# Kernel optimization log

Measured on AMD Instinct MI355X. Metric: run time of the kernel, lower is better.

The kernel has to match this reference:

```python
import jax, jax.numpy as jnp
import numpy as np

BS, T, FIN, FOUT = 8, 1024, 512, 512
ALPHA = 0.1      # leaky relu slope
T_K = 3          # t_ksize (odd); temporal band radius = T_K // 2
S_K = 4          # s_ksize semantic topk
NEG_INF = -9e15


def setup_inputs() -> dict:
    key = jax.random.key(0)
    k1, k2, k3, k4 = jax.random.split(key, 4)
    # xavier-uniform-ish scales (gain 1.414)
    w_lim = 1.414 * np.sqrt(6.0 / (FIN + FOUT))
    a_lim = 1.414 * np.sqrt(6.0 / (2 * FOUT + 1))
    return {
        "x_a": jax.random.normal(k1, (BS, T, FIN), jnp.float32),
        "x_v": jax.random.normal(k2, (BS, T, FIN), jnp.float32),
        "W": jax.random.uniform(k3, (FIN, FOUT), jnp.float32, -w_lim, w_lim),
        "a": jax.random.uniform(k4, (2 * FOUT, 1), jnp.float32, -a_lim, a_lim),
    }


def _temporal_mask(t):
    # tem_adj[i,j] = 1 iff |i-j| <= T_K//2 and i, j on the same side of t-0.5
    idx = jnp.arange(2 * t)
    same_side = (idx[:, None] >= t) == (idx[None, :] >= t)
    band = jnp.abs(idx[:, None] - idx[None, :]) <= (T_K // 2)
    return band & same_side  # (2t, 2t) bool


def _semantic_block_mask(x, k):
    # x: (bs, t, d). Top-k neighbors by negative squared euclidean distance.
    inner = 2.0 * jnp.einsum("btd,bsd->bts", x, x)
    sq = jnp.sum(x * x, axis=-1, keepdims=True)  # (bs, t, 1)
    pd = -(sq - inner + jnp.swapaxes(sq, -1, -2))  # (bs, t, t)
    _, idx = jax.lax.top_k(pd, k)  # (bs, t, k)
    bs, t = x.shape[0], x.shape[1]
    b_ix = jnp.arange(bs)[:, None, None]
    r_ix = jnp.arange(t)[None, :, None]
    return jnp.zeros((bs, t, t), bool).at[b_ix, r_ix, idx].set(True)


def reference(x_a, x_v, W, a):
    bs, t, _ = x_a.shape
    h = jnp.concatenate([x_a, x_v], axis=1)          # (bs, 2t, FIN)
    Wh = h @ W                                        # (bs, 2t, FOUT)

    # additive GAT score: e = leakyrelu(Wh a1 + (Wh a2)^T)
    Wh1 = Wh @ a[:FOUT]                               # (bs, 2t, 1)
    Wh2 = Wh @ a[FOUT:]                               # (bs, 2t, 1)
    e = Wh1 + jnp.swapaxes(Wh2, -1, -2)               # (bs, 2t, 2t)
    e = jnp.where(e > 0, e, ALPHA * e)                # leaky relu

    # adjacency: temporal band + semantic topk within aa / vv blocks
    tem = _temporal_mask(t)                           # (2t, 2t)
    sem_aa = _semantic_block_mask(Wh[:, :t], S_K)     # (bs, t, t)
    sem_vv = _semantic_block_mask(Wh[:, t:], S_K)     # (bs, t, t)
    zb = jnp.zeros((bs, t, t), bool)
    sem = jnp.concatenate([
        jnp.concatenate([sem_aa, zb], axis=-1),
        jnp.concatenate([zb, sem_vv], axis=-1),
    ], axis=1)                                        # (bs, 2t, 2t)
    mask = tem[None] | sem

    attention = jax.nn.softmax(jnp.where(mask, e, NEG_INF), axis=-1)
    h_prime = jax.nn.elu(attention @ Wh)              # (bs, 2t, FOUT)
    return h_prime[:, :t], h_prime[:, t:]
```

## Files before the change

### kernel.cpp

```cpp
#include <hip/hip_runtime.h>
#include <math.h>

#define T_ 1024
#define BS_ 8
#define D_ 512
#define NROWS_ (BS_*2*T_)
#define ALPHA_ 0.1f

typedef _Float16 f16;
typedef _Float16 f16x8 __attribute__((ext_vector_type(8)));
typedef _Float16 f16x4 __attribute__((ext_vector_type(4)));
typedef float f32x4 __attribute__((ext_vector_type(4)));

#define MFMA16(A,B,C) __builtin_amdgcn_mfma_f32_16x16x32_f16((A),(B),(C),0,0,0)

__device__ __forceinline__ void gl16(const void* g, void* l) {
    __builtin_amdgcn_global_load_lds(
        (const __attribute__((address_space(1))) unsigned int*)g,
        (__attribute__((address_space(3))) unsigned int*)l, 16, 0, 0);
}

__device__ __forceinline__ unsigned sortable(float f) {
    unsigned u = __float_as_uint(f);
    return u ^ ((u & 0x80000000u) ? 0xFFFFFFFFu : 0x80000000u);
}
__device__ __forceinline__ unsigned pack_key(float s, int col) {
    return (sortable(s) & 0xFFFFFC00u) | (unsigned)(1023 - col);
}

#define INSK4(K, X) { \
    bool g3 = (X) > K[3], g2 = (X) > K[2], g1 = (X) > K[1], g0 = (X) > K[0]; \
    K[3] = g2 ? K[2] : (g3 ? (X) : K[3]); \
    K[2] = g1 ? K[1] : (g2 ? (X) : K[2]); \
    K[1] = g0 ? K[0] : (g1 ? (X) : K[1]); \
    K[0] = g0 ? (X) : K[0]; }

#define INSK8(K, X) { \
    bool h7=(X)>K[7],h6=(X)>K[6],h5=(X)>K[5],h4=(X)>K[4]; \
    bool h3=(X)>K[3],h2=(X)>K[2],h1=(X)>K[1],h0=(X)>K[0]; \
    K[7]=h6?K[6]:(h7?(X):K[7]); K[6]=h5?K[5]:(h6?(X):K[6]); \
    K[5]=h4?K[4]:(h5?(X):K[5]); K[4]=h3?K[3]:(h4?(X):K[4]); \
    K[3]=h2?K[2]:(h3?(X):K[3]); K[2]=h1?K[1]:(h2?(X):K[2]); \
    K[1]=h0?K[0]:(h1?(X):K[1]); K[0]=h0?(X):K[0]; }

#define CEU(a,b) { unsigned mx_ = (a) > (b) ? (a) : (b); \
    unsigned mn_ = (a) > (b) ? (b) : (a); (a) = mx_; (b) = mn_; }

#define MERGE8(K, MSK) { \
    unsigned b0=__shfl_xor(K[0],MSK), b1=__shfl_xor(K[1],MSK), \
             b2=__shfl_xor(K[2],MSK), b3=__shfl_xor(K[3],MSK), \
             b4=__shfl_xor(K[4],MSK), b5=__shfl_xor(K[5],MSK), \
             b6=__shfl_xor(K[6],MSK), b7=__shfl_xor(K[7],MSK); \
    K[0]=K[0]>b7?K[0]:b7; K[1]=K[1]>b6?K[1]:b6; \
    K[2]=K[2]>b5?K[2]:b5; K[3]=K[3]>b4?K[3]:b4; \
    K[4]=K[4]>b3?K[4]:b3; K[5]=K[5]>b2?K[5]:b2; \
    K[6]=K[6]>b1?K[6]:b1; K[7]=K[7]>b0?K[7]:b0; \
    CEU(K[0],K[4]); CEU(K[1],K[5]); CEU(K[2],K[6]); CEU(K[3],K[7]); \
    CEU(K[0],K[2]); CEU(K[1],K[3]); CEU(K[4],K[6]); CEU(K[5],K[7]); \
    CEU(K[0],K[1]); CEU(K[2],K[3]); CEU(K[4],K[5]); CEU(K[6],K[7]); }

#define BETTER(x,xi,v,vi) ((x) > (v) || ((x) == (v) && (xi) < (vi)))
#define INS4T(TV,TI,X,ID) { \
    bool g3 = BETTER(X,ID,TV[3],TI[3]), g2 = BETTER(X,ID,TV[2],TI[2]); \
    bool g1 = BETTER(X,ID,TV[1],TI[1]), g0 = BETTER(X,ID,TV[0],TI[0]); \
    TV[3] = g2 ? TV[2] : (g3 ? (X) : TV[3]); TI[3] = g2 ? TI[2] : (g3 ? (ID) : TI[3]); \
    TV[2] = g1 ? TV[1] : (g2 ? (X) : TV[2]); TI[2] = g1 ? TI[1] : (g2 ? (ID) : TI[2]); \
    TV[1] = g0 ? TV[0] : (g1 ? (X) : TV[1]); TI[1] = g0 ? TI[0] : (g1 ? (ID) : TI[1]); \
    TV[0] = g0 ? (X) : TV[0]; TI[0] = g0 ? (ID) : TI[0]; }

__global__ __launch_bounds__(256) void k_splitW(
    const float* __restrict__ W, f16* __restrict__ WTh, f16* __restrict__ WTl)
{
    __shared__ float tile[64][65];
    const int tid = threadIdx.x;
    const int tk = (blockIdx.x >> 3) << 6, tn = (blockIdx.x & 7) << 6;
    const int r0 = tid >> 4, c4 = (tid & 15) << 2;

    #pragma unroll
    for (int rr = 0; rr < 4; ++rr) {
        int k = r0 + (rr << 4);
        float4 v = *(const float4*)(W + (size_t)(tk + k) * D_ + tn + c4);
        tile[k][c4+0] = v.x; tile[k][c4+1] = v.y;
        tile[k][c4+2] = v.z; tile[k][c4+3] = v.w;
    }
    __syncthreads();
    #pragma unroll
    for (int rr = 0; rr < 4; ++rr) {
        int n = r0 + (rr << 4);
        f16x4 h, l;
        #pragma unroll
        for (int i = 0; i < 4; ++i) {
            float x = tile[c4 + i][n];
            f16 hh = (f16)x; h[i] = hh; l[i] = (f16)(x - (float)hh);
        }
        *(f16x4*)(WTh + (size_t)(tn + n) * D_ + tk + c4) = h;
        *(f16x4*)(WTl + (size_t)(tn + n) * D_ + tk + c4) = l;
    }
}

#define SA_OFF 73728
#define ST_OFF 77824
__global__ __launch_bounds__(256) void k_gemm_wh(
    const float* __restrict__ xa, const float* __restrict__ xv,
    const f16* __restrict__ WTh, const f16* __restrict__ WTl,
    const float* __restrict__ a,
    f16* __restrict__ Whh, f16* __restrict__ Whl,
    float* __restrict__ Wh1, float* __restrict__ Wh2, float* __restrict__ sq)
{
    __shared__ __align__(16) unsigned char smem[79360];

    const int tid  = threadIdx.x;
    const int w    = tid >> 6;
    const int lane = tid & 63;
    const int l15  = lane & 15;
    const int g    = lane >> 4;
    const int rowbase = blockIdx.x << 5;

    const int r8  = lane >> 3;
    const int k7  = lane & 7;
    const int sw2 = ((k7 ^ r8) << 4);
    const int rowA = tid >> 3;
    const int k7A  = tid & 7;
    const int aswz = ((k7A ^ (rowA & 7)) << 4);

    const int q0x = (((lane >> 4) ^ (lane & 7)) << 4);
    const int aoff0 = 65536 + ((0  + l15) << 7) + q0x;
    const int aoff1 = 65536 + ((16 + l15) << 7) + q0x;
    const int boff0 = (((w << 6) +  0 + l15) << 7) + q0x;
    const int boff1 = (((w << 6) + 16 + l15) << 7) + q0x;
    const int boff2 = (((w << 6) + 32 + l15) << 7) + q0x;
    const int boff3 = (((w << 6) + 48 + l15) << 7) + q0x;

    *(float4*)(smem + SA_OFF + (tid << 4)) = *(const float4*)(a + (tid << 2));

    const int qp = rowbase >> 10;
    const float* srcA = ((qp & 1) ? xv : xa)
                      + (size_t)((qp >> 1) * 1024 + (rowbase & 1023) + rowA) * D_ + (k7A << 3);

    const char* WThB = (const char*)WTh;
    const char* WTlB = (const char*)WTl;

    float st1[8], st2[8], stq[8];
    #pragma unroll
    for (int s = 0; s < 8; ++s) { st1[s] = 0.f; st2[s] = 0.f; stq[s] = 0.f; }

    for (int ct = 0; ct < 2; ++ct) {
        const int colbase = ct << 8;
        f32x4 acc[2][4];
        #pragma unroll
        for (int m = 0; m < 2; ++m)
            #pragma unroll
            for (int c = 0; c < 4; ++c) acc[m][c] = (f32x4){0.f,0.f,0.f,0.f};

        for (int kc = 0; kc < 8; ++kc) {
            size_t gB = ((size_t)(colbase + (w << 6) + r8) << 10) + (kc << 7) + sw2;
            int ldsB = (w << 13) + (lane << 4);
            #pragma unroll
            for (int j = 0; j < 8; ++j) {
                gl16(WThB + gB, smem + ldsB);
                gl16(WTlB + gB, smem + 32768 + ldsB);
                gB += (size_t)8 << 10; ldsB += 1024;
            }
            {
                float4 v0 = *(const float4*)(srcA + (kc << 6));
                float4 v1 = *(const float4*)(srcA + (kc << 6) + 4);
                float xs[8] = {v0.x,v0.y,v0.z,v0.w,v1.x,v1.y,v1.z,v1.w};
                f16x8 hi, lo;
                #pragma unroll
                for (int e = 0; e < 8; ++e) {
                    f16 h = (f16)xs[e]; hi[e] = h; lo[e] = (f16)(xs[e] - (float)h);
                }
                const int ldsA = 65536 + (rowA << 7) + aswz;
                *(f16x8*)(smem + ldsA)        = hi;
                *(f16x8*)(smem + ldsA + 4096) = lo;
            }
            __syncthreads();

            #pragma unroll
            for (int s = 0; s < 2; ++s) {
                const int sx = s << 6;
                f16x8 ah0 = *(const f16x8*)(smem + (aoff0 ^ sx));
                f16x8 ah1 = *(const f16x8*)(smem + (aoff1 ^ sx));
                f16x8 al0 = *(const f16x8*)(smem + ((aoff0 ^ sx) + 4096));
                f16x8 al1 = *(const f16x8*)(smem + ((aoff1 ^ sx) + 4096));
                f16x8 bh0 = *(const f16x8*)(smem + (boff0 ^ sx));
                f16x8 bh1 = *(const f16x8*)(smem + (boff1 ^ sx));
                f16x8 bh2 = *(const f16x8*)(smem + (boff2 ^ sx));
                f16x8 bh3 = *(const f16x8*)(smem + (boff3 ^ sx));
                f16x8 bl0 = *(const f16x8*)(smem + ((boff0 ^ sx) + 32768));
                f16x8 bl1 = *(const f16x8*)(smem + ((boff1 ^ sx) + 32768));
                f16x8 bl2 = *(const f16x8*)(smem + ((boff2 ^ sx) + 32768));
                f16x8 bl3 = *(const f16x8*)(smem + ((boff3 ^ sx) + 32768));

                acc[0][0] = MFMA16(ah0, bh0, acc[0][0]);
                acc[0][1] = MFMA16(ah0, bh1, acc[0][1]);
                acc[0][2] = MFMA16(ah0, bh2, acc[0][2]);
                acc[0][3] = MFMA16(ah0, bh3, acc[0][3]);
                acc[1][0] = MFMA16(ah1, bh0, acc[1][0]);
                acc[1][1] = MFMA16(ah1, bh1, acc[1][1]);
                acc[1][2] = MFMA16(ah1, bh2, acc[1][2]);
                acc[1][3] = MFMA16(ah1, bh3, acc[1][3]);
                acc[0][0] = MFMA16(al0, bh0, acc[0][0]);
                acc[0][1] = MFMA16(al0, bh1, acc[0][1]);
                acc[0][2] = MFMA16(al0, bh2, acc[0][2]);
                acc[0][3] = MFMA16(al0, bh3, acc[0][3]);
                acc[1][0] = MFMA16(al1, bh0, acc[1][0]);
                acc[1][1] = MFMA16(al1, bh1, acc[1][1]);
                acc[1][2] = MFMA16(al1, bh2, acc[1][2]);
                acc[1][3] = MFMA16(al1, bh3, acc[1][3]);
                acc[0][0] = MFMA16(ah0, bl0, acc[0][0]);
                acc[0][1] = MFMA16(ah0, bl1, acc[0][1]);
                acc[0][2] = MFMA16(ah0, bl2, acc[0][2]);
                acc[0][3] = MFMA16(ah0, bl3, acc[0][3]);
                acc[1][0] = MFMA16(ah1, bl0, acc[1][0]);
                acc[1][1] = MFMA16(ah1, bl1, acc[1][1]);
                acc[1][2] = MFMA16(ah1, bl2, acc[1][2]);
                acc[1][3] = MFMA16(ah1, bl3, acc[1][3]);
            }
            __syncthreads();
        }

        #pragma unroll
        for (int c = 0; c < 4; ++c) {
            const int col = (ct << 8) + (w << 6) + (c << 4) + l15;
            const float a1 = *(const float*)(smem + SA_OFF + (col << 2));
            const float a2 = *(const float*)(smem + SA_OFF + 2048 + (col << 2));
            #pragma unroll
            for (int m = 0; m < 2; ++m)
                #pragma unroll
                for (int j = 0; j < 4; ++j) {
                    const float v = acc[m][c][j];
                    const int slot = (m << 2) + j;
                    st1[slot] = fmaf(v, a1, st1[slot]);
                    st2[slot] = fmaf(v, a2, st2[slot]);
                    stq[slot] = fmaf(v, v,  stq[slot]);
                    f16 h = (f16)v; f16 l = (f16)(v - (float)h);
                    const size_t off = (size_t)(rowbase + (m << 4) + (g << 2) + j) * D_ + col;
                    Whh[off] = h; Whl[off] = l;
                }
        }
    }

    #pragma unroll
    for (int mask = 1; mask < 16; mask <<= 1)
        #pragma unroll
        for (int s = 0; s < 8; ++s) {
            st1[s] += __shfl_xor(st1[s], mask);
            st2[s] += __shfl_xor(st2[s], mask);
            stq[s] += __shfl_xor(stq[s], mask);
        }
    if (l15 == 0) {
        #pragma unroll
        for (int s = 0; s < 8; ++s) {
            const int rl = ((s >> 2) << 4) + (g << 2) + (s & 3);
            float* sp = (float*)(smem + ST_OFF) + ((w << 5) + rl) * 3;
            sp[0] = st1[s]; sp[1] = st2[s]; sp[2] = stq[s];
        }
    }
    __syncthreads();
    if (tid < 32) {
        float s1 = 0.f, s2 = 0.f, s3 = 0.f;
        #pragma unroll
        for (int wv = 0; wv < 4; ++wv) {
            const float* sp = (const float*)(smem + ST_OFF) + ((wv << 5) + tid) * 3;
            s1 += sp[0]; s2 += sp[1]; s3 += sp[2];
        }
        Wh1[rowbase + tid] = s1; Wh2[rowbase + tid] = s2; sq[rowbase + tid] = s3;
    }
}

__global__ __launch_bounds__(512, 1) void k_gram_topk8(
    const f16* __restrict__ Whh, const float* __restrict__ sq,
    int* __restrict__ topk8)
{
    __shared__ __align__(16) unsigned char smem[81920];

    const int bid = blockIdx.x;
    const int swz = ((bid & 7) << 5) + (bid >> 3);
    const int p   = swz >> 4;
    const int rt  = swz & 15;
    const int rowbase  = (p << 10) + (rt << 6);
    const int colPanel = p << 10;

    const int tid  = threadIdx.x;
    const int w    = tid >> 6;
    const int wr   = w >> 2, wc = w & 3;
    const int lane = tid & 63;
    const int l15  = lane & 15;
    const int g    = lane >> 4;
    const int r8   = lane >> 3;
    const int k7   = lane & 7;
    const int sw2  = ((k7 ^ r8) << 4);
    const int q0x  = ((g ^ (lane & 7)) << 4);

    const int rowA = tid >> 3;
    const int k7A  = tid & 7;
    const int aswz = ((k7A ^ (rowA & 7)) << 4);

    const char* WB = (const char*)Whh;

    const int aoff0 = 32768 + (((wr << 5) +  0 + l15) << 7) + q0x;
    const int aoff1 = 32768 + (((wr << 5) + 16 + l15) << 7) + q0x;
    const int boff0 = (((wc << 6) +  0 + l15) << 7) + q0x;
    const int boff1 = (((wc << 6) + 16 + l15) << 7) + q0x;
    const int boff2 = (((wc << 6) + 32 + l15) << 7) + q0x;
    const int boff3 = (((wc << 6) + 48 + l15) << 7) + q0x;

    f32x4 acc[2][4];
    #pragma unroll
    for (int m = 0; m < 2; ++m)
        #pragma unroll
        for (int c = 0; c < 4; ++c) acc[m][c] = (f32x4){0.f,0.f,0.f,0.f};

    unsigned k4[8][4];
    #pragma unroll
    for (int s = 0; s < 8; ++s)
        #pragma unroll
        for (int q = 0; q < 4; ++q) k4[s][q] = 0u;

    #define STAGE_G(t) { \
        const int ct_ = (t) >> 3, kc_ = (t) & 7; \
        const int bufb_ = ((t) & 1) * 40960; \
        size_t gB_ = ((size_t)(colPanel + (ct_ << 8) + (w << 5) + r8) << 10) + (kc_ << 7) + sw2; \
        int ldsB_ = bufb_ + (w << 12) + (lane << 4); \
        _Pragma("unroll") \
        for (int j_ = 0; j_ < 4; ++j_) { \
            gl16(WB + gB_, smem + ldsB_); \
            gB_ += (size_t)8 << 10; ldsB_ += 1024; \
        } \
        size_t gA_ = ((size_t)(rowbase + rowA) << 10) + (kc_ << 7) + aswz; \
        gl16(WB + gA_, smem + bufb_ + 32768 + (tid << 4)); \
    }

    STAGE_G(0);

    for (int t = 0; t < 32; ++t) {
        __syncthreads();
        if (t < 31) STAGE_G(t + 1);
        const int bufb = (t & 1) * 40960;

        #pragma unroll
        for (int s = 0; s < 2; ++s) {
            const int sx = s << 6;
            f16x8 a0 = *(const f16x8*)(smem + bufb + (aoff0 ^ sx));
            f16x8 a1 = *(const f16x8*)(smem + bufb + (aoff1 ^ sx));
            f16x8 b0 = *(const f16x8*)(smem + bufb + (boff0 ^ sx));
            f16x8 b1 = *(const f16x8*)(smem + bufb + (boff1 ^ sx));
            f16x8 b2 = *(const f16x8*)(smem + bufb + (boff2 ^ sx));
            f16x8 b3 = *(const f16x8*)(smem + bufb + (boff3 ^ sx));
            acc[0][0] = MFMA16(a0, b0, acc[0][0]);
            acc[0][1] = MFMA16(a0, b1, acc[0][1]);
            acc[0][2] = MFMA16(a0, b2, acc[0][2]);
            acc[0][3] = MFMA16(a0, b3, acc[0][3]);
            acc[1][0] = MFMA16(a1, b0, acc[1][0]);
            acc[1][1] = MFMA16(a1, b1, acc[1][1]);
            acc[1][2] = MFMA16(a1, b2, acc[1][2]);
            acc[1][3] = MFMA16(a1, b3, acc[1][3]);
        }

        if ((t & 7) == 7) {
            const int ct = t >> 3;
            #pragma unroll
            for (int c = 0; c < 4; ++c) {
                const int cl = (ct << 8) + (wc << 6) + (c << 4) + l15;
                const float sqc = sq[colPanel + cl];
                #pragma unroll
                for (int m = 0; m < 2; ++m)
                    #pragma unroll
                    for (int j = 0; j < 4; ++j) {
                        float sc = fmaf(2.f, acc[m][c][j], -sqc);
                        unsigned key = pack_key(sc, cl);
                        INSK4(k4[(m << 2) + j], key);
                    }
                acc[0][c] = (f32x4){0.f,0.f,0.f,0.f};
                acc[1][c] = (f32x4){0.f,0.f,0.f,0.f};
            }
        }
    }

    unsigned k8[8][8];
    #pragma unroll
    for (int s = 0; s < 8; ++s) {
        #pragma unroll
        for (int q = 0; q < 4; ++q) { k8[s][q] = k4[s][q]; k8[s][4 + q] = 0u; }
    }
    #pragma unroll
    for (int msk = 1; msk < 16; msk <<= 1) {
        #pragma unroll
        for (int s = 0; s < 8; ++s) { MERGE8(k8[s], msk); }
    }

    if (l15 == 0) {
        #pragma unroll
        for (int s = 0; s < 8; ++s) {
            const int row_local = ((s >> 2) << 4) + (g << 2) + (s & 3);
            const int off = ((((wr << 5) + row_local) << 2) + wc) << 5;
            *(uint4*)(smem + off)      = make_uint4(k8[s][0], k8[s][1], k8[s][2], k8[s][3]);
            *(uint4*)(smem + off + 16) = make_uint4(k8[s][4], k8[s][5], k8[s][6], k8[s][7]);
        }
    }
    __syncthreads();
    if (tid < 64) {
        const unsigned* bp = (const unsigned*)smem + (tid << 5);
        unsigned kk[8];
        #pragma unroll
        for (int s = 0; s < 8; ++s) kk[s] = bp[s];
        #pragma unroll
        for (int wv = 1; wv < 4; ++wv)
            #pragma unroll
            for (int s = 0; s < 8; ++s) { unsigned x = bp[(wv << 3) + s]; INSK8(kk, x); }
        #pragma unroll
        for (int s = 0; s < 8; ++s)
            topk8[(((size_t)(rowbase + tid)) << 3) + s] = 1023 - (int)(kk[s] & 1023u);
    }
    #undef STAGE_G
}

__global__ __launch_bounds__(256) void k_rescore_agg(
    const f16* __restrict__ Whh, const f16* __restrict__ Whl,
    const float* __restrict__ Wh1, const float* __restrict__ Wh2,
    const float* __restrict__ sq, const int* __restrict__ topk8,
    float* __restrict__ out)
{
    const int bid = blockIdx.x;
    const int swz = ((bid & 7) << 9) + (bid >> 3);
    const int tid  = threadIdx.x;
    const int lane = tid & 63;
    const int r    = (swz << 2) + (tid >> 6);
    const int p    = r >> 10;
    const int i    = r & 1023;
    const int rb   = p << 10;

    const size_t ro = (size_t)r * D_ + (lane << 3);
    f16x8 ah = *(const f16x8*)(Whh + ro);
    f16x8 al = *(const f16x8*)(Whl + ro);
    float av[8];
    #pragma unroll
    for (int e = 0; e < 8; ++e) av[e] = (float)ah[e] + (float)al[e];

    int cid[8];
    {
        int4 t0 = *(const int4*)(topk8 + ((size_t)r << 3));
        int4 t1 = *(const int4*)(topk8 + ((size_t)r << 3) + 4);
        cid[0]=t0.x; cid[1]=t0.y; cid[2]=t0.z; cid[3]=t0.w;
        cid[4]=t1.x; cid[5]=t1.y; cid[6]=t1.z; cid[7]=t1.w;
    }

    float dp[8];
    #pragma unroll
    for (int c = 0; c < 8; ++c) {
        const size_t co = (size_t)(rb + cid[c]) * D_ + (lane << 3);
        f16x8 bh = *(const f16x8*)(Whh + co);
        f16x8 bl = *(const f16x8*)(Whl + co);
        float s = 0.f;
        #pragma unroll
        for (int e = 0; e < 8; ++e)
            s = fmaf(av[e], (float)bh[e] + (float)bl[e], s);
        dp[c] = s;
    }
    #pragma unroll
    for (int off = 32; off > 0; off >>= 1)
        #pragma unroll
        for (int c = 0; c < 8; ++c) dp[c] += __shfl_xor(dp[c], off);

    float tv[4] = {-3.4e38f,-3.4e38f,-3.4e38f,-3.4e38f};
    int   ti[4] = {0x7FFFFFFF,0x7FFFFFFF,0x7FFFFFFF,0x7FFFFFFF};
    #pragma unroll
    for (int c = 0; c < 8; ++c) {
        float sc = fmaf(2.f, dp[c], -sq[rb + cid[c]]);
        INS4T(tv, ti, sc, cid[c]);
    }

    const int  tM = i - 1, tC = i, tP = i + 1;
    const bool vM = (i > 0), vP = (i < T_ - 1);
    const int s0 = ti[0], s1 = ti[1], s2 = ti[2], s3 = ti[3];

    bool u0 = !((vM && s0 == tM) || (s0 == tC) || (vP && s0 == tP));
    bool u1 = !((vM && s1 == tM) || (s1 == tC) || (vP && s1 == tP));
    bool u2 = !((vM && s2 == tM) || (s2 == tC) || (vP && s2 == tP));
    bool u3 = !((vM && s3 == tM) || (s3 == tC) || (vP && s3 == tP));

    int  ci[7] = { vM ? tM : 0, tC, vP ? tP : 0, s0, s1, s2, s3 };
    bool cv[7] = { vM, true, vP, u0, u1, u2, u3 };

    const float e1 = Wh1[r];
    float ev[7];
    float m = -3.4e38f;
    #pragma unroll
    for (int q = 0; q < 7; ++q) {
        float e = e1 + Wh2[rb + ci[q]];
        e = (e > 0.f) ? e : ALPHA_ * e;
        e = cv[q] ? e : -3.4e38f;
        ev[q] = e;
        m = fmaxf(m, e);
    }
    float wsum = 0.f;
    #pragma unroll
    for (int q = 0; q < 7; ++q) {
        float wq = cv[q] ? expf(ev[q] - m) : 0.f;
        ev[q] = wq;
        wsum += wq;
    }
    #pragma unroll
    for (int q = 0; q < 7; ++q) ev[q] /= wsum;

    float A[8] = {0.f,0.f,0.f,0.f,0.f,0.f,0.f,0.f};
    #pragma unroll
    for (int q = 0; q < 7; ++q) {
        if (ev[q] > 0.f) {
            const float wq = ev[q];
            const size_t qo = (size_t)(rb + ci[q]) * D_ + (lane << 3);
            f16x8 vh = *(const f16x8*)(Whh + qo);
            f16x8 vl = *(const f16x8*)(Whl + qo);
            #pragma unroll
            for (int e = 0; e < 8; ++e)
                A[e] = fmaf(wq, (float)vh[e] + (float)vl[e], A[e]);
        }
    }
    #pragma unroll
    for (int e = 0; e < 8; ++e)
        A[e] = (A[e] > 0.f) ? A[e] : expm1f(A[e]);

    const int blk = p & 1, b = p >> 1;
    float* dst = out + (size_t)blk * ((size_t)BS_ * T_ * D_)
               + ((size_t)((b << 10) + i)) * D_ + (lane << 3);
    *(float4*)(dst)     = make_float4(A[0], A[1], A[2], A[3]);
    *(float4*)(dst + 4) = make_float4(A[4], A[5], A[6], A[7]);
}

extern "C" void kernel_launch(void* const* d_in, const int* in_sizes, int n_in,
                              void* d_out, int out_size, void* d_ws, size_t ws_size,
                              hipStream_t stream)
{
    const float* xa = (const float*)d_in[0];
    const float* xv = (const float*)d_in[1];
    const float* W  = (const float*)d_in[2];
    const float* a  = (const float*)d_in[3];
    float* out = (float*)d_out;

    f16* Whh    = (f16*)d_ws;
    f16* Whl    = Whh + (size_t)NROWS_ * D_;
    f16* WTh    = Whl + (size_t)NROWS_ * D_;
    f16* WTl    = WTh + (size_t)D_ * D_;
    float* Wh1  = (float*)(WTl + (size_t)D_ * D_);
    float* Wh2  = Wh1 + NROWS_;
    float* sq   = Wh2 + NROWS_;
    int* topk8  = (int*)(sq + NROWS_);

    k_splitW     <<<dim3(64),   dim3(256), 0, stream>>>(W, WTh, WTl);
    k_gemm_wh    <<<dim3(512),  dim3(256), 0, stream>>>(xa, xv, WTh, WTl, a, Whh, Whl, Wh1, Wh2, sq);
    k_gram_topk8 <<<dim3(256),  dim3(512), 0, stream>>>(Whh, sq, topk8);
    k_rescore_agg<<<dim3(4096), dim3(256), 0, stream>>>(Whh, Whl, Wh1, Wh2, sq, topk8, out);
}
```

Measured before the change: 128.8 us.

## Double-buffer W tiles and keep activation fragments in registers in the projection GEMM

```diff
diff --git a/kernel.cpp b/kernel.cpp
--- a/kernel.cpp
+++ b/kernel.cpp
@@ -98,148 +98,166 @@
     }
 }
 
-#define SA_OFF 73728
-#define ST_OFF 77824
-__global__ __launch_bounds__(256) void k_gemm_wh(
+__global__ __launch_bounds__(512, 2) void k_gemm_wh(
     const float* __restrict__ xa, const float* __restrict__ xv,
     const f16* __restrict__ WTh, const f16* __restrict__ WTl,
     const float* __restrict__ a,
     f16* __restrict__ Whh, f16* __restrict__ Whl,
     float* __restrict__ Wh1, float* __restrict__ Wh2, float* __restrict__ sq)
 {
-    __shared__ __align__(16) unsigned char smem[79360];
+    __shared__ __align__(16) unsigned char smem[135168];
 
     const int tid  = threadIdx.x;
     const int w    = tid >> 6;
+    const int wr   = w >> 2, wc = w & 3;
     const int lane = tid & 63;
     const int l15  = lane & 15;
     const int g    = lane >> 4;
-    const int rowbase = blockIdx.x << 5;
-
-    const int r8  = lane >> 3;
-    const int k7  = lane & 7;
-    const int sw2 = ((k7 ^ r8) << 4);
-    const int rowA = tid >> 3;
-    const int k7A  = tid & 7;
-    const int aswz = ((k7A ^ (rowA & 7)) << 4);
-
-    const int q0x = (((lane >> 4) ^ (lane & 7)) << 4);
-    const int aoff0 = 65536 + ((0  + l15) << 7) + q0x;
-    const int aoff1 = 65536 + ((16 + l15) << 7) + q0x;
-    const int boff0 = (((w << 6) +  0 + l15) << 7) + q0x;
-    const int boff1 = (((w << 6) + 16 + l15) << 7) + q0x;
-    const int boff2 = (((w << 6) + 32 + l15) << 7) + q0x;
-    const int boff3 = (((w << 6) + 48 + l15) << 7) + q0x;
-
-    *(float4*)(smem + SA_OFF + (tid << 4)) = *(const float4*)(a + (tid << 2));
+    const int r8   = lane >> 3;
+    const int k7   = lane & 7;
+    const int sw2  = ((k7 ^ r8) << 4);
+    const int q0x  = ((g ^ (lane & 7)) << 4);
+    const int rowbase = blockIdx.x << 6;
+
+    if (tid < 256)
+        *(float4*)(smem + 131072 + (tid << 4)) = *(const float4*)(a + (tid << 2));
 
     const int qp = rowbase >> 10;
-    const float* srcA = ((qp & 1) ? xv : xa)
-                      + (size_t)((qp >> 1) * 1024 + (rowbase & 1023) + rowA) * D_ + (k7A << 3);
+    const float* xsrc = ((qp & 1) ? xv : xa)
+                      + (size_t)((qp >> 1) * 1024 + (rowbase & 1023)) * D_;
+    const int arow = (wr << 5) + l15;
 
     const char* WThB = (const char*)WTh;
     const char* WTlB = (const char*)WTl;
 
-    float st1[8], st2[8], stq[8];
-    #pragma unroll
-    for (int s = 0; s < 8; ++s) { st1[s] = 0.f; st2[s] = 0.f; stq[s] = 0.f; }
-
-    for (int ct = 0; ct < 2; ++ct) {
-        const int colbase = ct << 8;
-        f32x4 acc[2][4];
+    const int bo0 = (((wc << 6) +  0 + l15) << 7) + q0x;
+    const int bo1 = (((wc << 6) + 16 + l15) << 7) + q0x;
+    const int bo2 = (((wc << 6) + 32 + l15) << 7) + q0x;
+    const int bo3 = (((wc << 6) + 48 + l15) << 7) + q0x;
+
+    #define STAGE_B(ct_, kc_, buf_) { \
+        size_t gB_ = ((size_t)(((ct_) << 8) + (w << 5) + r8) << 10) + ((kc_) << 7) + sw2; \
+        int ldsB_ = (buf_) * 65536 + (w << 12) + (lane << 4); \
+        _Pragma("unroll") \
+        for (int j_ = 0; j_ < 4; ++j_) { \
+            gl16(WThB + gB_, smem + ldsB_); \
+            gl16(WTlB + gB_, smem + 32768 + ldsB_); \
+            gB_ += (size_t)8 << 10; ldsB_ += 1024; } }
+
+    #define LOAD_A(dst_, kc_) { \
+        _Pragma("unroll") \
+        for (int r_ = 0; r_ < 2; ++r_) { \
+            const float* p_ = xsrc + (size_t)(arow + (r_ << 4)) * D_ + ((kc_) << 6) + (g << 3); \
+            dst_[(r_ << 2) + 0] = *(const float4*)(p_); \
+            dst_[(r_ << 2) + 1] = *(const float4*)(p_ + 4); \
+            dst_[(r_ << 2) + 2] = *(const float4*)(p_ + 32); \
+            dst_[(r_ << 2) + 3] = *(const float4*)(p_ + 36); } }
+
+    #define CONV_A(src_) { \
+        _Pragma("unroll") \
+        for (int r_ = 0; r_ < 2; ++r_) \
+        _Pragma("unroll") \
+        for (int s_ = 0; s_ < 2; ++s_) { \
+            float4 v0_ = src_[(r_ << 2) + (s_ << 1)]; \
+            float4 v1_ = src_[(r_ << 2) + (s_ << 1) + 1]; \
+            float xs_[8] = {v0_.x,v0_.y,v0_.z,v0_.w,v1_.x,v1_.y,v1_.z,v1_.w}; \
+            f16x8 h_, l_; \
+            _Pragma("unroll") \
+            for (int e_ = 0; e_ < 8; ++e_) { \
+                f16 hh_ = (f16)xs_[e_]; h_[e_] = hh_; l_[e_] = (f16)(xs_[e_] - (float)hh_); } \
+            AH[r_][s_] = h_; AL[r_][s_] = l_; } }
+
+    f32x4 acc[2][2][4];
+    #pragma unroll
+    for (int ct = 0; ct < 2; ++ct)
         #pragma unroll
         for (int m = 0; m < 2; ++m)
             #pragma unroll
-            for (int c = 0; c < 4; ++c) acc[m][c] = (f32x4){0.f,0.f,0.f,0.f};
-
-        for (int kc = 0; kc < 8; ++kc) {
-            size_t gB = ((size_t)(colbase + (w << 6) + r8) << 10) + (kc << 7) + sw2;
-            int ldsB = (w << 13) + (lane << 4);
-            #pragma unroll
-            for (int j = 0; j < 8; ++j) {
-                gl16(WThB + gB, smem + ldsB);
-                gl16(WTlB + gB, smem + 32768 + ldsB);
-                gB += (size_t)8 << 10; ldsB += 1024;
-            }
-            {
-                float4 v0 = *(const float4*)(srcA + (kc << 6));
-                float4 v1 = *(const float4*)(srcA + (kc << 6) + 4);
-                float xs[8] = {v0.x,v0.y,v0.z,v0.w,v1.x,v1.y,v1.z,v1.w};
-                f16x8 hi, lo;
-                #pragma unroll
-                for (int e = 0; e < 8; ++e) {
-                    f16 h = (f16)xs[e]; hi[e] = h; lo[e] = (f16)(xs[e] - (float)h);
-                }
-                const int ldsA = 65536 + (rowA << 7) + aswz;
-                *(f16x8*)(smem + ldsA)        = hi;
-                *(f16x8*)(smem + ldsA + 4096) = lo;
-            }
-            __syncthreads();
-
-            #pragma unroll
-            for (int s = 0; s < 2; ++s) {
-                const int sx = s << 6;
-                f16x8 ah0 = *(const f16x8*)(smem + (aoff0 ^ sx));
-                f16x8 ah1 = *(const f16x8*)(smem + (aoff1 ^ sx));
-                f16x8 al0 = *(const f16x8*)(smem + ((aoff0 ^ sx) + 4096));
-                f16x8 al1 = *(const f16x8*)(smem + ((aoff1 ^ sx) + 4096));
-                f16x8 bh0 = *(const f16x8*)(smem + (boff0 ^ sx));
-                f16x8 bh1 = *(const f16x8*)(smem + (boff1 ^ sx));
-                f16x8 bh2 = *(const f16x8*)(smem + (boff2 ^ sx));
-                f16x8 bh3 = *(const f16x8*)(smem + (boff3 ^ sx));
-                f16x8 bl0 = *(const f16x8*)(smem + ((boff0 ^ sx) + 32768));
-                f16x8 bl1 = *(const f16x8*)(smem + ((boff1 ^ sx) + 32768));
-                f16x8 bl2 = *(const f16x8*)(smem + ((boff2 ^ sx) + 32768));
-                f16x8 bl3 = *(const f16x8*)(smem + ((boff3 ^ sx) + 32768));
-
-                acc[0][0] = MFMA16(ah0, bh0, acc[0][0]);
-                acc[0][1] = MFMA16(ah0, bh1, acc[0][1]);
-                acc[0][2] = MFMA16(ah0, bh2, acc[0][2]);
-                acc[0][3] = MFMA16(ah0, bh3, acc[0][3]);
-                acc[1][0] = MFMA16(ah1, bh0, acc[1][0]);
-                acc[1][1] = MFMA16(ah1, bh1, acc[1][1]);
-                acc[1][2] = MFMA16(ah1, bh2, acc[1][2]);
-                acc[1][3] = MFMA16(ah1, bh3, acc[1][3]);
-                acc[0][0] = MFMA16(al0, bh0, acc[0][0]);
-                acc[0][1] = MFMA16(al0, bh1, acc[0][1]);
-                acc[0][2] = MFMA16(al0, bh2, acc[0][2]);
-                acc[0][3] = MFMA16(al0, bh3, acc[0][3]);
-                acc[1][0] = MFMA16(al1, bh0, acc[1][0]);
-                acc[1][1] = MFMA16(al1, bh1, acc[1][1]);
-                acc[1][2] = MFMA16(al1, bh2, acc[1][2]);
-                acc[1][3] = MFMA16(al1, bh3, acc[1][3]);
-                acc[0][0] = MFMA16(ah0, bl0, acc[0][0]);
-                acc[0][1] = MFMA16(ah0, bl1, acc[0][1]);
-                acc[0][2] = MFMA16(ah0, bl2, acc[0][2]);
-                acc[0][3] = MFMA16(ah0, bl3, acc[0][3]);
-                acc[1][0] = MFMA16(ah1, bl0, acc[1][0]);
-                acc[1][1] = MFMA16(ah1, bl1, acc[1][1]);
-                acc[1][2] = MFMA16(ah1, bl2, acc[1][2]);
-                acc[1][3] = MFMA16(ah1, bl3, acc[1][3]);
-            }
-            __syncthreads();
-        }
-
+            for (int c = 0; c < 4; ++c) acc[ct][m][c] = (f32x4){0.f,0.f,0.f,0.f};
+
+    float4 aR[8];
+    f16x8 AH[2][2], AL[2][2];
+
+    LOAD_A(aR, 0);
+    STAGE_B(0, 0, 0);
+
+    #pragma unroll
+    for (int t = 0; t < 16; ++t) {
+        const int kc = t >> 1, ct = t & 1, bufb = (t & 1) * 65536;
+        __syncthreads();
+        if (t < 15) STAGE_B((t + 1) & 1, (t + 1) >> 1, (t + 1) & 1);
+        if (ct == 0) { CONV_A(aR); }
+        else if (kc < 7) { LOAD_A(aR, kc + 1); }
+
+        #pragma unroll
+        for (int s = 0; s < 2; ++s) {
+            const int sx = s << 6;
+            f16x8 bh0 = *(const f16x8*)(smem + bufb + (bo0 ^ sx));
+            f16x8 bh1 = *(const f16x8*)(smem + bufb + (bo1 ^ sx));
+            f16x8 bh2 = *(const f16x8*)(smem + bufb + (bo2 ^ sx));
+            f16x8 bh3 = *(const f16x8*)(smem + bufb + (bo3 ^ sx));
+            f16x8 bl0 = *(const f16x8*)(smem + bufb + 32768 + (bo0 ^ sx));
+            f16x8 bl1 = *(const f16x8*)(smem + bufb + 32768 + (bo1 ^ sx));
+            f16x8 bl2 = *(const f16x8*)(smem + bufb + 32768 + (bo2 ^ sx));
+            f16x8 bl3 = *(const f16x8*)(smem + bufb + 32768 + (bo3 ^ sx));
+
+            acc[ct][0][0] = MFMA16(AH[0][s], bh0, acc[ct][0][0]);
+            acc[ct][0][1] = MFMA16(AH[0][s], bh1, acc[ct][0][1]);
+            acc[ct][0][2] = MFMA16(AH[0][s], bh2, acc[ct][0][2]);
+            acc[ct][0][3] = MFMA16(AH[0][s], bh3, acc[ct][0][3]);
+            acc[ct][1][0] = MFMA16(AH[1][s], bh0, acc[ct][1][0]);
+            acc[ct][1][1] = MFMA16(AH[1][s], bh1, acc[ct][1][1]);
+            acc[ct][1][2] = MFMA16(AH[1][s], bh2, acc[ct][1][2]);
+            acc[ct][1][3] = MFMA16(AH[1][s], bh3, acc[ct][1][3]);
+            acc[ct][0][0] = MFMA16(AL[0][s], bh0, acc[ct][0][0]);
+            acc[ct][0][1] = MFMA16(AL[0][s], bh1, acc[ct][0][1]);
+            acc[ct][0][2] = MFMA16(AL[0][s], bh2, acc[ct][0][2]);
+            acc[ct][0][3] = MFMA16(AL[0][s], bh3, acc[ct][0][3]);
+            acc[ct][1][0] = MFMA16(AL[1][s], bh0, acc[ct][1][0]);
+            acc[ct][1][1] = MFMA16(AL[1][s], bh1, acc[ct][1][1]);
+            acc[ct][1][2] = MFMA16(AL[1][s], bh2, acc[ct][1][2]);
+            acc[ct][1][3] = MFMA16(AL[1][s], bh3, acc[ct][1][3]);
+            acc[ct][0][0] = MFMA16(AH[0][s], bl0, acc[ct][0][0]);
+            acc[ct][0][1] = MFMA16(AH[0][s], bl1, acc[ct][0][1]);
+            acc[ct][0][2] = MFMA16(AH[0][s], bl2, acc[ct][0][2]);
+            acc[ct][0][3] = MFMA16(AH[0][s], bl3, acc[ct][0][3]);
+            acc[ct][1][0] = MFMA16(AH[1][s], bl0, acc[ct][1][0]);
+            acc[ct][1][1] = MFMA16(AH[1][s], bl1, acc[ct][1][1]);
+            acc[ct][1][2] = MFMA16(AH[1][s], bl2, acc[ct][1][2]);
+            acc[ct][1][3] = MFMA16(AH[1][s], bl3, acc[ct][1][3]);
+        }
+    }
+    #undef STAGE_B
+    #undef LOAD_A
+    #undef CONV_A
+
+    __syncthreads();
+
+    float st1[8], st2[8], stq[8];
+    #pragma unroll
+    for (int s = 0; s < 8; ++s) { st1[s] = 0.f; st2[s] = 0.f; stq[s] = 0.f; }
+
+    #pragma unroll
+    for (int ct = 0; ct < 2; ++ct)
         #pragma unroll
         for (int c = 0; c < 4; ++c) {
-            const int col = (ct << 8) + (w << 6) + (c << 4) + l15;
-            const float a1 = *(const float*)(smem + SA_OFF + (col << 2));
-            const float a2 = *(const float*)(smem + SA_OFF + 2048 + (col << 2));
+            const int col = (ct << 8) + (wc << 6) + (c << 4) + l15;
+            const float a1 = *(const float*)(smem + 131072 + (col << 2));
+            const float a2 = *(const float*)(smem + 131072 + 2048 + (col << 2));
             #pragma unroll
             for (int m = 0; m < 2; ++m)
                 #pragma unroll
                 for (int j = 0; j < 4; ++j) {
-                    const float v = acc[m][c][j];
+                    const float v = acc[ct][m][c][j];
                     const int slot = (m << 2) + j;
                     st1[slot] = fmaf(v, a1, st1[slot]);
                     st2[slot] = fmaf(v, a2, st2[slot]);
                     stq[slot] = fmaf(v, v,  stq[slot]);
                     f16 h = (f16)v; f16 l = (f16)(v - (float)h);
-                    const size_t off = (size_t)(rowbase + (m << 4) + (g << 2) + j) * D_ + col;
+                    const size_t off = (size_t)(rowbase + (wr << 5) + (m << 4) + (g << 2) + j) * D_ + col;
                     Whh[off] = h; Whl[off] = l;
                 }
         }
-    }
 
     #pragma unroll
     for (int mask = 1; mask < 16; mask <<= 1)
@@ -252,17 +270,17 @@
     if (l15 == 0) {
         #pragma unroll
         for (int s = 0; s < 8; ++s) {
-            const int rl = ((s >> 2) << 4) + (g << 2) + (s & 3);
-            float* sp = (float*)(smem + ST_OFF) + ((w << 5) + rl) * 3;
+            const int rl = (wr << 5) + ((s >> 2) << 4) + (g << 2) + (s & 3);
+            float* sp = (float*)smem + ((rl << 2) + wc) * 3;
             sp[0] = st1[s]; sp[1] = st2[s]; sp[2] = stq[s];
         }
     }
     __syncthreads();
-    if (tid < 32) {
+    if (tid < 64) {
         float s1 = 0.f, s2 = 0.f, s3 = 0.f;
         #pragma unroll
         for (int wv = 0; wv < 4; ++wv) {
-            const float* sp = (const float*)(smem + ST_OFF) + ((wv << 5) + tid) * 3;
+            const float* sp = (const float*)smem + ((tid << 2) + wv) * 3;
             s1 += sp[0]; s2 += sp[1]; s3 += sp[2];
         }
         Wh1[rowbase + tid] = s1; Wh2[rowbase + tid] = s2; sq[rowbase + tid] = s3;
@@ -548,7 +566,7 @@
     int* topk8  = (int*)(sq + NROWS_);
 
     k_splitW     <<<dim3(64),   dim3(256), 0, stream>>>(W, WTh, WTl);
-    k_gemm_wh    <<<dim3(512),  dim3(256), 0, stream>>>(xa, xv, WTh, WTl, a, Whh, Whl, Wh1, Wh2, sq);
+    k_gemm_wh    <<<dim3(256),  dim3(512), 0, stream>>>(xa, xv, WTh, WTl, a, Whh, Whl, Wh1, Wh2, sq);
     k_gram_topk8 <<<dim3(256),  dim3(512), 0, stream>>>(Whh, sq, topk8);
     k_rescore_agg<<<dim3(4096), dim3(256), 0, stream>>>(Whh, Whl, Wh1, Wh2, sq, topk8, out);
 }
```

Measured after the change: 126.6 us. Within noise of the previous version (-1.8%).
